# Kernel tuning notes

Measured on AMD Instinct MI355X. Metric: run time of the kernel, lower is better.

The kernel has to match this reference:

```python
import jax, jax.numpy as jnp
import numpy as np

N = 50000      # num nodes
E = 800000     # num edges
D = 128        # num_hid
EPS = 1e-8


def _mlp(x, w1, b1, w2, b2):
    # 2-layer MLP: Linear -> ReLU -> Linear (dropout disabled at inference)
    return jax.nn.relu(x @ w1 + b1) @ w2 + b2


def setup_inputs() -> dict:
    key = jax.random.key(0)
    ks = jax.random.split(key, 12)

    def lin(k, fan_in, fan_out):
        kw, kb = jax.random.split(k)
        lim = 1.0 / np.sqrt(fan_in)
        w = jax.random.uniform(kw, (fan_in, fan_out), jnp.float32, -lim, lim)
        b = jax.random.uniform(kb, (fan_out,), jnp.float32, -lim, lim)
        return w, b

    H = jax.random.normal(ks[0], (N, D), jnp.float32)
    edge_index = jax.random.randint(ks[1], (2, E), 0, N, jnp.int64)
    w1_1, b1_1 = lin(ks[2], 2 * D, D)   # mlp_1 layer 1
    w1_2, b1_2 = lin(ks[3], D, D)       # mlp_1 layer 2
    w2_1, b2_1 = lin(ks[4], 2 * D, D)   # mlp_2 layer 1
    w2_2, b2_2 = lin(ks[5], D, 1)       # mlp_2 layer 2 (channel_curv=False -> out=1)
    t = jnp.zeros((), jnp.float32)
    return {"t": t, "H": H, "edge_index": edge_index,
            "w1_1": w1_1, "b1_1": b1_1, "w1_2": w1_2, "b1_2": b1_2,
            "w2_1": w2_1, "b2_1": b2_1, "w2_2": w2_2, "b2_2": b2_2}


def reference(t, H, edge_index, w1_1, b1_1, w1_2, b1_2, w2_1, b2_1, w2_2, b2_2):
    src, dst = edge_index[0], edge_index[1]

    # damping: row-normalize H
    H = H / (jnp.linalg.norm(H, axis=1, keepdims=True) + EPS)

    H_i = H[src]                                    # [E, D]
    H_j = H[dst]                                    # [E, D]

    # curvature(H_i, H_j)
    c = jnp.concatenate((H_i, H_j), axis=1)         # [E, 2D]
    c = jax.nn.relu(_mlp(c, w1_1, b1_1, w1_2, b1_2))  # [E, D]
    c = jax.ops.segment_sum(c, src, num_segments=N)   # scatter-sum -> [N, D]
    c = jnp.concatenate((c[src], c[dst]), axis=1)     # [E, 2D]
    curv = _mlp(c, w2_1, b2_1, w2_2, b2_2)            # [E, 1]

    # damped edge message
    cos = jnp.sum(H_i * H_j, axis=1, keepdims=True)   # [E, 1]
    H_edge = curv * (H_j - cos * H_i)                 # [E, D]

    # scatter-mean over source node
    s = jax.ops.segment_sum(H_edge, src, num_segments=N)               # [N, D]
    cnt = jax.ops.segment_sum(jnp.ones((E, 1), H.dtype), src, num_segments=N)
    Hm = s / jnp.maximum(cnt, 1.0)

    # damping: row-normalize output
    return Hm / (jnp.linalg.norm(Hm, axis=1, keepdims=True) + EPS)
```

## Files before the change

### kernel.cpp

```cpp
#include <hip/hip_runtime.h>
#include <hip/hip_bf16.h>

#define D 128
#define EPS 1e-8f
#define E1S 136

typedef _Float16 f16;
typedef __attribute__((ext_vector_type(8))) _Float16 half8;
typedef __attribute__((ext_vector_type(4))) float f32x4;
typedef unsigned int uint;

__device__ inline float2 up2(uint u) {
    union { uint u; f16 h[2]; } v; v.u = u;
    return make_float2((float)v.h[0], (float)v.h[1]);
}

__global__ void k_normalize(const float* __restrict__ H, f16* __restrict__ Hn, int N) {
    int row = blockIdx.x * 4 + (threadIdx.x >> 6);
    int lane = threadIdx.x & 63;
    if (row >= N) return;
    float2 v = reinterpret_cast<const float2*>(H + (size_t)row * D)[lane];
    float ss = v.x * v.x + v.y * v.y;
    #pragma unroll
    for (int off = 32; off; off >>= 1) ss += __shfl_xor(ss, off, 64);
    float scale = 1.0f / (sqrtf(ss) + EPS);
    union { f16 h[2]; uint u; } p;
    p.h[0] = (f16)(v.x * scale);
    p.h[1] = (f16)(v.y * scale);
    reinterpret_cast<uint*>(Hn + (size_t)row * D)[lane] = p.u;
}

__global__ void k_hist(const int* __restrict__ src, int* __restrict__ deg, int E) {
    for (int e = blockIdx.x * blockDim.x + threadIdx.x; e < E; e += gridDim.x * blockDim.x)
        atomicAdd(&deg[src[e]], 1);
}

__global__ void k_scan(const int* __restrict__ deg, int* __restrict__ rowptr, int N) {
    __shared__ int wsum[16];
    __shared__ int carry;
    int t = threadIdx.x, lane = t & 63, w = t >> 6;
    if (t == 0) carry = 0;
    __syncthreads();
    for (int base = 0; base < N; base += 4096) {
        int i0 = base + t * 4;
        int a = 0, b = 0, c = 0, d = 0;
        if (i0 + 3 < N) {
            int4 v4 = *reinterpret_cast<const int4*>(deg + i0);
            a = v4.x; b = v4.y; c = v4.z; d = v4.w;
        } else {
            if (i0 < N) a = deg[i0];
            if (i0 + 1 < N) b = deg[i0 + 1];
            if (i0 + 2 < N) c = deg[i0 + 2];
            if (i0 + 3 < N) d = deg[i0 + 3];
        }
        int s1 = a + b, s2 = s1 + c, s3 = s2 + d;
        int v = s3;
        #pragma unroll
        for (int off = 1; off < 64; off <<= 1) {
            int u = __shfl_up(v, off, 64);
            if (lane >= off) v += u;
        }
        if (lane == 63) wsum[w] = v;
        __syncthreads();
        if (w == 0 && lane < 16) {
            int s = wsum[lane];
            #pragma unroll
            for (int off = 1; off < 16; off <<= 1) {
                int u = __shfl_up(s, off, 64);
                if (lane >= off) s += u;
            }
            wsum[lane] = s;
        }
        __syncthreads();
        int add = (w > 0 ? wsum[w - 1] : 0) + carry;
        int incl = v + add;
        int pre = incl - s3;
        if (i0 < N)     rowptr[i0 + 1] = pre + a;
        if (i0 + 1 < N) rowptr[i0 + 2] = pre + s1;
        if (i0 + 2 < N) rowptr[i0 + 3] = pre + s2;
        if (i0 + 3 < N) rowptr[i0 + 4] = pre + s3;
        __syncthreads();
        if (t == 1023) carry = incl;
        __syncthreads();
    }
    if (t == 0) rowptr[0] = 0;
}

__global__ void k_scatter(const int* __restrict__ src, const int* __restrict__ dst,
                          const int* __restrict__ rowptr, int* __restrict__ fill,
                          int* __restrict__ srcS, int* __restrict__ dstS, int E) {
    for (int e = blockIdx.x * blockDim.x + threadIdx.x; e < E; e += gridDim.x * blockDim.x) {
        int s = src[e];
        int pos = atomicAdd(&fill[s], 1);
        int idx = rowptr[s] + pos;
        srcS[idx] = s;
        dstS[idx] = dst[e];
    }
}

__global__ void k_prep_all(const float* __restrict__ w1_1, const float* __restrict__ w1_2,
                           const float* __restrict__ w2_1, f16* __restrict__ Wt) {
    int b = blockIdx.x;
    int m = b >> 6;
    int idx = (b & 63) * 256 + threadIdx.x;
    int k = idx >> 7, n = idx & 127;
    const float* W = (m == 0) ? w1_1
                   : (m == 1) ? w1_1 + 16384
                   : (m == 2) ? w1_2
                   : (m == 3) ? w2_1
                              : w2_1 + 16384;
    Wt[m * 16384 + n * 128 + k] = (f16)W[k * 128 + n];
}

template <bool A_F16>
__global__ __launch_bounds__(256, 4)
void k_gemm_dual(const void* __restrict__ Aptr, const f16* __restrict__ Wt0,
                 const f16* __restrict__ Wt1, const float* __restrict__ bias0,
                 f16* __restrict__ out0, f16* __restrict__ out1, int N) {
    __shared__ f16 As[64 * E1S];
    int t = threadIdx.x;
    int r0 = blockIdx.x * 64;
    int l = t & 63, w = t >> 6, n0 = w * 32;
    {
        int er = t >> 2, kb = (t & 3) * 32;
        int rc = min(r0 + er, N - 1);
        if (A_F16) {
            const half8* Ap = reinterpret_cast<const half8*>((const f16*)Aptr + (size_t)rc * 128 + kb);
            #pragma unroll
            for (int q = 0; q < 4; ++q)
                *reinterpret_cast<half8*>(&As[er * E1S + kb + q * 8]) = Ap[q];
        } else {
            const float4* Ap = reinterpret_cast<const float4*>((const float*)Aptr + (size_t)rc * 128 + kb);
            #pragma unroll
            for (int q = 0; q < 4; ++q) {
                float4 a0 = Ap[q * 2], a1 = Ap[q * 2 + 1];
                half8 sv;
                sv[0] = (f16)a0.x; sv[1] = (f16)a0.y; sv[2] = (f16)a0.z; sv[3] = (f16)a0.w;
                sv[4] = (f16)a1.x; sv[5] = (f16)a1.y; sv[6] = (f16)a1.z; sv[7] = (f16)a1.w;
                *reinterpret_cast<half8*>(&As[er * E1S + kb + q * 8]) = sv;
            }
        }
    }
    half8 bfrag[2][4];
    #pragma unroll
    for (int nt = 0; nt < 2; ++nt) {
        int col = n0 + nt * 16 + (l & 15);
        #pragma unroll
        for (int kt = 0; kt < 4; ++kt)
            bfrag[nt][kt] = *reinterpret_cast<const half8*>(Wt0 + col * 128 + kt * 32 + (l >> 4) * 8);
    }
    float b0a = bias0[n0 + (l & 15)];
    float b0b = bias0[n0 + 16 + (l & 15)];
    __syncthreads();
    f32x4 acc0[4][2], acc1[4][2];
    #pragma unroll
    for (int mt = 0; mt < 4; ++mt) {
        acc0[mt][0] = (f32x4){0,0,0,0}; acc0[mt][1] = (f32x4){0,0,0,0};
        acc1[mt][0] = (f32x4){0,0,0,0}; acc1[mt][1] = (f32x4){0,0,0,0};
    }
    #pragma unroll
    for (int mt = 0; mt < 4; ++mt) {
        int arow = mt * 16 + (l & 15);
        #pragma unroll
        for (int kt = 0; kt < 4; ++kt) {
            half8 af = *reinterpret_cast<const half8*>(&As[arow * E1S + kt * 32 + (l >> 4) * 8]);
            acc0[mt][0] = __builtin_amdgcn_mfma_f32_16x16x32_f16(af, bfrag[0][kt], acc0[mt][0], 0, 0, 0);
            acc0[mt][1] = __builtin_amdgcn_mfma_f32_16x16x32_f16(af, bfrag[1][kt], acc0[mt][1], 0, 0, 0);
        }
    }
    #pragma unroll
    for (int nt = 0; nt < 2; ++nt) {
        int col = n0 + nt * 16 + (l & 15);
        #pragma unroll
        for (int kt = 0; kt < 4; ++kt)
            bfrag[nt][kt] = *reinterpret_cast<const half8*>(Wt1 + col * 128 + kt * 32 + (l >> 4) * 8);
    }
    #pragma unroll
    for (int mt = 0; mt < 4; ++mt) {
        int arow = mt * 16 + (l & 15);
        #pragma unroll
        for (int kt = 0; kt < 4; ++kt) {
            half8 af = *reinterpret_cast<const half8*>(&As[arow * E1S + kt * 32 + (l >> 4) * 8]);
            acc1[mt][0] = __builtin_amdgcn_mfma_f32_16x16x32_f16(af, bfrag[0][kt], acc1[mt][0], 0, 0, 0);
            acc1[mt][1] = __builtin_amdgcn_mfma_f32_16x16x32_f16(af, bfrag[1][kt], acc1[mt][1], 0, 0, 0);
        }
    }
    __syncthreads();
    #pragma unroll
    for (int mt = 0; mt < 4; ++mt)
        #pragma unroll
        for (int j = 0; j < 4; ++j) {
            int row = mt * 16 + (l >> 4) * 4 + j;
            As[row * E1S + n0 + (l & 15)]      = (f16)(acc0[mt][0][j] + b0a);
            As[row * E1S + n0 + 16 + (l & 15)] = (f16)(acc0[mt][1][j] + b0b);
        }
    __syncthreads();
    {
        int er = t >> 2, kb = (t & 3) * 32;
        int row = r0 + er;
        if (row < N)
            #pragma unroll
            for (int q = 0; q < 4; ++q)
                *reinterpret_cast<half8*>(out0 + (size_t)row * 128 + kb + q * 8) =
                    *reinterpret_cast<const half8*>(&As[er * E1S + kb + q * 8]);
    }
    __syncthreads();
    #pragma unroll
    for (int mt = 0; mt < 4; ++mt)
        #pragma unroll
        for (int j = 0; j < 4; ++j) {
            int row = mt * 16 + (l >> 4) * 4 + j;
            As[row * E1S + n0 + (l & 15)]      = (f16)acc1[mt][0][j];
            As[row * E1S + n0 + 16 + (l & 15)] = (f16)acc1[mt][1][j];
        }
    __syncthreads();
    {
        int er = t >> 2, kb = (t & 3) * 32;
        int row = r0 + er;
        if (row < N)
            #pragma unroll
            for (int q = 0; q < 4; ++q)
                *reinterpret_cast<half8*>(out1 + (size_t)row * 128 + kb + q * 8) =
                    *reinterpret_cast<const half8*>(&As[er * E1S + kb + q * 8]);
    }
}

__global__ __launch_bounds__(256, 5)
void k_edge_mlp1(const int* __restrict__ srcS, const int* __restrict__ dstS,
                 const int* __restrict__ rowptr,
                 const f16* __restrict__ P, const f16* __restrict__ Q,
                 const f16* __restrict__ Wt, const float* __restrict__ b1_2,
                 float* __restrict__ C, int E) {
    __shared__ f16 e1s[64 * E1S];
    int t = threadIdx.x;
    int e0 = blockIdx.x * 64;
    int l = t & 63, w = t >> 6, n0 = w * 32;
    {
        int er = t >> 2, kb = (t & 3) * 32;
        int ge = min(e0 + er, E - 1);
        int sc = srcS[ge], dj = dstS[ge];
        const half8* Pp = reinterpret_cast<const half8*>(P + (size_t)sc * 128 + kb);
        const half8* Qp = reinterpret_cast<const half8*>(Q + (size_t)dj * 128 + kb);
        #pragma unroll
        for (int q = 0; q < 4; ++q) {
            half8 sv = Pp[q] + Qp[q];
            #pragma unroll
            for (int i = 0; i < 8; ++i)
                sv[i] = sv[i] > (f16)0 ? sv[i] : (f16)0;
            *reinterpret_cast<half8*>(&e1s[er * E1S + kb + q * 8]) = sv;
        }
    }
    half8 bfrag[2][4];
    #pragma unroll
    for (int nt = 0; nt < 2; ++nt) {
        int col = n0 + nt * 16 + (l & 15);
        #pragma unroll
        for (int kt = 0; kt < 4; ++kt)
            bfrag[nt][kt] = *reinterpret_cast<const half8*>(Wt + col * 128 + kt * 32 + (l >> 4) * 8);
    }
    float bias0 = b1_2[n0 + (l & 15)];
    float bias1 = b1_2[n0 + 16 + (l & 15)];
    __syncthreads();
    f32x4 acc[4][2];
    #pragma unroll
    for (int mt = 0; mt < 4; ++mt) { acc[mt][0] = (f32x4){0,0,0,0}; acc[mt][1] = (f32x4){0,0,0,0}; }
    #pragma unroll
    for (int mt = 0; mt < 4; ++mt) {
        int arow = mt * 16 + (l & 15);
        #pragma unroll
        for (int kt = 0; kt < 4; ++kt) {
            half8 af = *reinterpret_cast<const half8*>(&e1s[arow * E1S + kt * 32 + (l >> 4) * 8]);
            acc[mt][0] = __builtin_amdgcn_mfma_f32_16x16x32_f16(af, bfrag[0][kt], acc[mt][0], 0, 0, 0);
            acc[mt][1] = __builtin_amdgcn_mfma_f32_16x16x32_f16(af, bfrag[1][kt], acc[mt][1], 0, 0, 0);
        }
    }
    #pragma unroll
    for (int mt = 0; mt < 4; ++mt)
        #pragma unroll
        for (int j = 0; j < 4; ++j) {
            acc[mt][0][j] = fmaxf(acc[mt][0][j] + bias0, 0.f);
            acc[mt][1][j] = fmaxf(acc[mt][1][j] + bias1, 0.f);
        }
    int myv = (e0 + l < E) ? srcS[e0 + l] : -1;
    int pv = __shfl_up(myv, 1, 64);
    bool head = (l == 0) || (myv != pv);
    unsigned long long validm = __ballot(myv >= 0);
    unsigned long long hm = __ballot(head) & validm;
    int nvalid = __popcll(validm);
    int grp = l >> 4;
    while (hm) {
        int lo = __builtin_ctzll(hm);
        hm &= hm - 1;
        int hi = hm ? __builtin_ctzll(hm) : nvalid;
        int s = __shfl(myv, lo, 64);
        float v0 = 0.f, v1 = 0.f;
        #pragma unroll
        for (int mt = 0; mt < 4; ++mt) {
            int tlo = mt * 16, thi = mt * 16 + 16;
            if (thi <= lo || tlo >= hi) continue;
            if (lo <= tlo && hi >= thi) {
                #pragma unroll
                for (int j = 0; j < 4; ++j) {
                    v0 += acc[mt][0][j];
                    v1 += acc[mt][1][j];
                }
            } else {
                #pragma unroll
                for (int j = 0; j < 4; ++j) {
                    int row = tlo + grp * 4 + j;
                    bool in = (row >= lo) && (row < hi);
                    v0 += in ? acc[mt][0][j] : 0.f;
                    v1 += in ? acc[mt][1][j] : 0.f;
                }
            }
        }
        v0 += __shfl_xor(v0, 16, 64); v0 += __shfl_xor(v0, 32, 64);
        v1 += __shfl_xor(v1, 16, 64); v1 += __shfl_xor(v1, 32, 64);
        if (l < 16) {
            int rs = rowptr[s], re = rowptr[s + 1];
            float* cp = C + (size_t)s * 128 + n0 + l;
            if (rs >= e0 && re <= e0 + 64) {
                cp[0] = v0; cp[16] = v1;
            } else {
                atomicAdd(cp, v0); atomicAdd(cp + 16, v1);
            }
        }
    }
}

__global__ void k_node_curv(const int* __restrict__ dstS, const int* __restrict__ rowptr,
                            const f16* __restrict__ Hn,
                            const f16* __restrict__ Rb, const f16* __restrict__ Tb,
                            const float* __restrict__ w2_2, const float* __restrict__ b2_2,
                            float* __restrict__ out, int N) {
    int node = blockIdx.x * 4 + (threadIdx.x >> 6);
    int lane = threadIdx.x & 63;
    if (node >= N) return;
    int sub = lane & 15;
    int slot = lane >> 4;
    const uint4* HnU = reinterpret_cast<const uint4*>(Hn);
    const uint4* TbU = reinterpret_cast<const uint4*>(Tb);
    uint4 hiu = HnU[(size_t)node * 16 + sub];
    uint4 rvu = reinterpret_cast<const uint4*>(Rb)[(size_t)node * 16 + sub];
    float hif[8], rvf[8], wvf[8];
    {
        const uint* hp = &hiu.x;
        const uint* rp = &rvu.x;
        float4 w0 = reinterpret_cast<const float4*>(w2_2)[sub * 2];
        float4 w1 = reinterpret_cast<const float4*>(w2_2)[sub * 2 + 1];
        #pragma unroll
        for (int k = 0; k < 4; ++k) {
            float2 h = up2(hp[k]); hif[k * 2] = h.x; hif[k * 2 + 1] = h.y;
            float2 r = up2(rp[k]); rvf[k * 2] = r.x; rvf[k * 2 + 1] = r.y;
        }
        wvf[0] = w0.x; wvf[1] = w0.y; wvf[2] = w0.z; wvf[3] = w0.w;
        wvf[4] = w1.x; wvf[5] = w1.y; wvf[6] = w1.z; wvf[7] = w1.w;
    }
    float bb = b2_2[0];
    int lo = rowptr[node], hiE = rowptr[node + 1];
    int deg = hiE - lo;
    float ax[8];
    #pragma unroll
    for (int j = 0; j < 8; ++j) ax[j] = 0.f;
    float sc = 0.f;
    int e = lo + slot;
    bool valid = e < hiE;
    int dcur = valid ? dstS[e] : 0;
    uint4 hju = HnU[(size_t)dcur * 16 + sub];
    uint4 tvu = TbU[(size_t)dcur * 16 + sub];
    for (int it = 0; it < deg; it += 4) {
        int e2 = lo + it + 4 + slot;
        bool valid2 = e2 < hiE;
        int d2 = valid2 ? dstS[e2] : 0;
        uint4 hjN = HnU[(size_t)d2 * 16 + sub];
        uint4 tvN = TbU[(size_t)d2 * 16 + sub];
        float hjf[8];
        float pcos = 0.f, pcur = 0.f;
        {
            const uint* hp = &hju.x;
            const uint* tp = &tvu.x;
            #pragma unroll
            for (int k = 0; k < 4; ++k) {
                float2 h = up2(hp[k]);
                float2 tv = up2(tp[k]);
                hjf[k * 2] = h.x; hjf[k * 2 + 1] = h.y;
                pcos += hif[k * 2] * h.x + hif[k * 2 + 1] * h.y;
                pcur += fmaxf(rvf[k * 2] + tv.x, 0.f) * wvf[k * 2]
                      + fmaxf(rvf[k * 2 + 1] + tv.y, 0.f) * wvf[k * 2 + 1];
            }
        }
        #pragma unroll
        for (int off = 1; off < 16; off <<= 1) {
            pcos += __shfl_xor(pcos, off, 64);
            pcur += __shfl_xor(pcur, off, 64);
        }
        float cur = valid ? (pcur + bb) : 0.f;
        #pragma unroll
        for (int j = 0; j < 8; ++j) ax[j] += cur * hjf[j];
        sc += cur * pcos;
        hju = hjN; tvu = tvN; valid = valid2;
    }
    #pragma unroll
    for (int j = 0; j < 8; ++j) {
        ax[j] += __shfl_xor(ax[j], 16, 64);
        ax[j] += __shfl_xor(ax[j], 32, 64);
    }
    sc += __shfl_xor(sc, 16, 64);
    sc += __shfl_xor(sc, 32, 64);
    float inv = 1.0f / fmaxf((float)deg, 1.0f);
    float ss = 0.f;
    #pragma unroll
    for (int j = 0; j < 8; ++j) {
        ax[j] = (ax[j] - sc * hif[j]) * inv;
        ss += ax[j] * ax[j];
    }
    #pragma unroll
    for (int off = 1; off < 16; off <<= 1) ss += __shfl_xor(ss, off, 64);
    float scale = 1.0f / (sqrtf(ss) + EPS);
    if (slot == 0) {
        float4 o0 = make_float4(ax[0] * scale, ax[1] * scale, ax[2] * scale, ax[3] * scale);
        float4 o1 = make_float4(ax[4] * scale, ax[5] * scale, ax[6] * scale, ax[7] * scale);
        float4* op = reinterpret_cast<float4*>(out + (size_t)node * 128 + sub * 8);
        op[0] = o0;
        op[1] = o1;
    }
}

extern "C" void kernel_launch(void* const* d_in, const int* in_sizes, int n_in,
                              void* d_out, int out_size, void* d_ws, size_t ws_size,
                              hipStream_t stream) {
    const float* H    = (const float*)d_in[1];
    const int*   ei   = (const int*)d_in[2];
    const float* w1_1 = (const float*)d_in[3];
    const float* b1_1 = (const float*)d_in[4];
    const float* w1_2 = (const float*)d_in[5];
    const float* b1_2 = (const float*)d_in[6];
    const float* w2_1 = (const float*)d_in[7];
    const float* b2_1 = (const float*)d_in[8];
    const float* w2_2 = (const float*)d_in[9];
    const float* b2_2 = (const float*)d_in[10];

    int N = in_sizes[1] / D;
    int E = in_sizes[2] / 2;
    const int* src = ei;
    const int* dst = ei + E;

    float* out = (float*)d_out;

    f16* Hnb    = (f16*)d_ws;
    f16* Pb     = Hnb + (size_t)N * D;
    f16* Qb     = Pb + (size_t)N * D;
    float* Cb   = (float*)(Qb + (size_t)N * D);
    f16* Wt     = (f16*)(Cb + (size_t)N * D);
    int* deg    = (int*)(Wt + 5 * 16384);
    int* rowptr = deg + N;
    int* fill   = rowptr + N + 1;
    int* srcS   = fill + N;
    int* dstS   = srcS + E;

    hipMemsetAsync(Cb, 0, (size_t)N * D * sizeof(float), stream);
    hipMemsetAsync(deg, 0, (3 * (size_t)N + 1) * sizeof(int), stream);

    k_normalize<<<(N + 3) / 4, 256, 0, stream>>>(H, Hnb, N);
    k_hist<<<1024, 256, 0, stream>>>(src, deg, E);
    k_scan<<<1, 1024, 0, stream>>>(deg, rowptr, N);
    k_scatter<<<1024, 256, 0, stream>>>(src, dst, rowptr, fill, srcS, dstS, E);
    k_prep_all<<<320, 256, 0, stream>>>(w1_1, w1_2, w2_1, Wt);

    k_gemm_dual<true><<<(N + 63) / 64, 256, 0, stream>>>(Hnb, Wt + 0 * 16384, Wt + 1 * 16384,
                                                         b1_1, Pb, Qb, N);
    k_edge_mlp1<<<(E + 63) / 64, 256, 0, stream>>>(srcS, dstS, rowptr, Pb, Qb,
                                                   Wt + 2 * 16384, b1_2, Cb, E);
    k_gemm_dual<false><<<(N + 63) / 64, 256, 0, stream>>>(Cb, Wt + 3 * 16384, Wt + 4 * 16384,
                                                          b2_1, Pb, Qb, N);
    k_node_curv<<<(N + 3) / 4, 256, 0, stream>>>(dstS, rowptr, Hnb, Pb, Qb, w2_2, b2_2, out, N);
}
```

Measured before the change: 352.4 us.

## Interleave normalized H with T rows and double-tile edge MLP blocks

Normalized H and the second-layer T projection are now stored interleaved in one 256-wide row buffer. The per-edge gather in k_node_curv can then fetch both halves for a destination node from one contiguous 512-byte region instead of two separate arrays. Separately, k_edge_mlp1 processes two 64-edge tiles per block, gathering the second tile into registers while the first is computed. This hides gather latency, at the cost of more registers and LDS and lower occupancy (launch bounds 5 to 4).

```diff
diff --git a/kernel.cpp b/kernel.cpp
--- a/kernel.cpp
+++ b/kernel.cpp
@@ -15,7 +15,7 @@
     return make_float2((float)v.h[0], (float)v.h[1]);
 }
 
-__global__ void k_normalize(const float* __restrict__ H, f16* __restrict__ Hn, int N) {
+__global__ void k_normalize(const float* __restrict__ H, f16* __restrict__ HT, int N) {
     int row = blockIdx.x * 4 + (threadIdx.x >> 6);
     int lane = threadIdx.x & 63;
     if (row >= N) return;
@@ -27,7 +27,7 @@
     union { f16 h[2]; uint u; } p;
     p.h[0] = (f16)(v.x * scale);
     p.h[1] = (f16)(v.y * scale);
-    reinterpret_cast<uint*>(Hn + (size_t)row * D)[lane] = p.u;
+    reinterpret_cast<uint*>(HT + (size_t)row * 256)[lane] = p.u;
 }
 
 __global__ void k_hist(const int* __restrict__ src, int* __restrict__ deg, int E) {
@@ -116,7 +116,8 @@
 __global__ __launch_bounds__(256, 4)
 void k_gemm_dual(const void* __restrict__ Aptr, const f16* __restrict__ Wt0,
                  const f16* __restrict__ Wt1, const float* __restrict__ bias0,
-                 f16* __restrict__ out0, f16* __restrict__ out1, int N) {
+                 f16* __restrict__ out0, f16* __restrict__ out1, int N,
+                 int astr, int o1str) {
     __shared__ f16 As[64 * E1S];
     int t = threadIdx.x;
     int r0 = blockIdx.x * 64;
@@ -125,12 +126,12 @@
         int er = t >> 2, kb = (t & 3) * 32;
         int rc = min(r0 + er, N - 1);
         if (A_F16) {
-            const half8* Ap = reinterpret_cast<const half8*>((const f16*)Aptr + (size_t)rc * 128 + kb);
+            const half8* Ap = reinterpret_cast<const half8*>((const f16*)Aptr + (size_t)rc * astr + kb);
             #pragma unroll
             for (int q = 0; q < 4; ++q)
                 *reinterpret_cast<half8*>(&As[er * E1S + kb + q * 8]) = Ap[q];
         } else {
-            const float4* Ap = reinterpret_cast<const float4*>((const float*)Aptr + (size_t)rc * 128 + kb);
+            const float4* Ap = reinterpret_cast<const float4*>((const float*)Aptr + (size_t)rc * astr + kb);
             #pragma unroll
             for (int q = 0; q < 4; ++q) {
                 float4 a0 = Ap[q * 2], a1 = Ap[q * 2 + 1];
@@ -220,24 +221,26 @@
         if (row < N)
             #pragma unroll
             for (int q = 0; q < 4; ++q)
-                *reinterpret_cast<half8*>(out1 + (size_t)row * 128 + kb + q * 8) =
+                *reinterpret_cast<half8*>(out1 + (size_t)row * o1str + kb + q * 8) =
                     *reinterpret_cast<const half8*>(&As[er * E1S + kb + q * 8]);
     }
 }
 
-__global__ __launch_bounds__(256, 5)
+__global__ __launch_bounds__(256, 4)
 void k_edge_mlp1(const int* __restrict__ srcS, const int* __restrict__ dstS,
                  const int* __restrict__ rowptr,
                  const f16* __restrict__ P, const f16* __restrict__ Q,
                  const f16* __restrict__ Wt, const float* __restrict__ b1_2,
                  float* __restrict__ C, int E) {
-    __shared__ f16 e1s[64 * E1S];
+    __shared__ f16 e1s[2 * 64 * E1S];
     int t = threadIdx.x;
-    int e0 = blockIdx.x * 64;
+    int e00 = blockIdx.x * 128;
+    int e01 = e00 + 64;
     int l = t & 63, w = t >> 6, n0 = w * 32;
+    int er = t >> 2, kb = (t & 3) * 32;
+
     {
-        int er = t >> 2, kb = (t & 3) * 32;
-        int ge = min(e0 + er, E - 1);
+        int ge = min(e00 + er, E - 1);
         int sc = srcS[ge], dj = dstS[ge];
         const half8* Pp = reinterpret_cast<const half8*>(P + (size_t)sc * 128 + kb);
         const half8* Qp = reinterpret_cast<const half8*>(Q + (size_t)dj * 128 + kb);
@@ -250,6 +253,21 @@
             *reinterpret_cast<half8*>(&e1s[er * E1S + kb + q * 8]) = sv;
         }
     }
+    half8 sv1[4];
+    {
+        int ge = min(e01 + er, E - 1);
+        int sc = srcS[ge], dj = dstS[ge];
+        const half8* Pp = reinterpret_cast<const half8*>(P + (size_t)sc * 128 + kb);
+        const half8* Qp = reinterpret_cast<const half8*>(Q + (size_t)dj * 128 + kb);
+        #pragma unroll
+        for (int q = 0; q < 4; ++q) {
+            half8 sv = Pp[q] + Qp[q];
+            #pragma unroll
+            for (int i = 0; i < 8; ++i)
+                sv[i] = sv[i] > (f16)0 ? sv[i] : (f16)0;
+            sv1[q] = sv;
+        }
+    }
     half8 bfrag[2][4];
     #pragma unroll
     for (int nt = 0; nt < 2; ++nt) {
@@ -260,77 +278,86 @@
     }
     float bias0 = b1_2[n0 + (l & 15)];
     float bias1 = b1_2[n0 + 16 + (l & 15)];
-    __syncthreads();
-    f32x4 acc[4][2];
-    #pragma unroll
-    for (int mt = 0; mt < 4; ++mt) { acc[mt][0] = (f32x4){0,0,0,0}; acc[mt][1] = (f32x4){0,0,0,0}; }
-    #pragma unroll
-    for (int mt = 0; mt < 4; ++mt) {
-        int arow = mt * 16 + (l & 15);
-        #pragma unroll
-        for (int kt = 0; kt < 4; ++kt) {
-            half8 af = *reinterpret_cast<const half8*>(&e1s[arow * E1S + kt * 32 + (l >> 4) * 8]);
-            acc[mt][0] = __builtin_amdgcn_mfma_f32_16x16x32_f16(af, bfrag[0][kt], acc[mt][0], 0, 0, 0);
-            acc[mt][1] = __builtin_amdgcn_mfma_f32_16x16x32_f16(af, bfrag[1][kt], acc[mt][1], 0, 0, 0);
-        }
-    }
-    #pragma unroll
-    for (int mt = 0; mt < 4; ++mt)
-        #pragma unroll
-        for (int j = 0; j < 4; ++j) {
-            acc[mt][0][j] = fmaxf(acc[mt][0][j] + bias0, 0.f);
-            acc[mt][1][j] = fmaxf(acc[mt][1][j] + bias1, 0.f);
-        }
-    int myv = (e0 + l < E) ? srcS[e0 + l] : -1;
-    int pv = __shfl_up(myv, 1, 64);
-    bool head = (l == 0) || (myv != pv);
-    unsigned long long validm = __ballot(myv >= 0);
-    unsigned long long hm = __ballot(head) & validm;
-    int nvalid = __popcll(validm);
-    int grp = l >> 4;
-    while (hm) {
-        int lo = __builtin_ctzll(hm);
-        hm &= hm - 1;
-        int hi = hm ? __builtin_ctzll(hm) : nvalid;
-        int s = __shfl(myv, lo, 64);
-        float v0 = 0.f, v1 = 0.f;
+
+    auto compute_tile = [&](const f16* buf, int ebase) {
+        f32x4 acc[4][2];
+        #pragma unroll
+        for (int mt = 0; mt < 4; ++mt) { acc[mt][0] = (f32x4){0,0,0,0}; acc[mt][1] = (f32x4){0,0,0,0}; }
         #pragma unroll
         for (int mt = 0; mt < 4; ++mt) {
-            int tlo = mt * 16, thi = mt * 16 + 16;
-            if (thi <= lo || tlo >= hi) continue;
-            if (lo <= tlo && hi >= thi) {
-                #pragma unroll
-                for (int j = 0; j < 4; ++j) {
-                    v0 += acc[mt][0][j];
-                    v1 += acc[mt][1][j];
+            int arow = mt * 16 + (l & 15);
+            #pragma unroll
+            for (int kt = 0; kt < 4; ++kt) {
+                half8 af = *reinterpret_cast<const half8*>(&buf[arow * E1S + kt * 32 + (l >> 4) * 8]);
+                acc[mt][0] = __builtin_amdgcn_mfma_f32_16x16x32_f16(af, bfrag[0][kt], acc[mt][0], 0, 0, 0);
+                acc[mt][1] = __builtin_amdgcn_mfma_f32_16x16x32_f16(af, bfrag[1][kt], acc[mt][1], 0, 0, 0);
+            }
+        }
+        #pragma unroll
+        for (int mt = 0; mt < 4; ++mt)
+            #pragma unroll
+            for (int j = 0; j < 4; ++j) {
+                acc[mt][0][j] = fmaxf(acc[mt][0][j] + bias0, 0.f);
+                acc[mt][1][j] = fmaxf(acc[mt][1][j] + bias1, 0.f);
+            }
+        int myv = (ebase + l < E) ? srcS[ebase + l] : -1;
+        int pvv = __shfl_up(myv, 1, 64);
+        bool head = (l == 0) || (myv != pvv);
+        unsigned long long validm = __ballot(myv >= 0);
+        unsigned long long hm = __ballot(head) & validm;
+        int nvalid = __popcll(validm);
+        int grp = l >> 4;
+        while (hm) {
+            int lo = __builtin_ctzll(hm);
+            hm &= hm - 1;
+            int hi = hm ? __builtin_ctzll(hm) : nvalid;
+            int s = __shfl(myv, lo, 64);
+            float v0 = 0.f, v1 = 0.f;
+            #pragma unroll
+            for (int mt = 0; mt < 4; ++mt) {
+                int tlo = mt * 16, thi = mt * 16 + 16;
+                if (thi <= lo || tlo >= hi) continue;
+                if (lo <= tlo && hi >= thi) {
+                    #pragma unroll
+                    for (int j = 0; j < 4; ++j) {
+                        v0 += acc[mt][0][j];
+                        v1 += acc[mt][1][j];
+                    }
+                } else {
+                    #pragma unroll
+                    for (int j = 0; j < 4; ++j) {
+                        int row = tlo + grp * 4 + j;
+                        bool in = (row >= lo) && (row < hi);
+                        v0 += in ? acc[mt][0][j] : 0.f;
+                        v1 += in ? acc[mt][1][j] : 0.f;
+                    }
                 }
-            } else {
-                #pragma unroll
-                for (int j = 0; j < 4; ++j) {
-                    int row = tlo + grp * 4 + j;
-                    bool in = (row >= lo) && (row < hi);
-                    v0 += in ? acc[mt][0][j] : 0.f;
-                    v1 += in ? acc[mt][1][j] : 0.f;
+            }
+            v0 += __shfl_xor(v0, 16, 64); v0 += __shfl_xor(v0, 32, 64);
+            v1 += __shfl_xor(v1, 16, 64); v1 += __shfl_xor(v1, 32, 64);
+            if (l < 16) {
+                int rs = rowptr[s], re = rowptr[s + 1];
+                float* cp = C + (size_t)s * 128 + n0 + l;
+                if (rs >= ebase && re <= ebase + 64) {
+                    cp[0] = v0; cp[16] = v1;
+                } else {
+                    atomicAdd(cp, v0); atomicAdd(cp + 16, v1);
                 }
             }
         }
-        v0 += __shfl_xor(v0, 16, 64); v0 += __shfl_xor(v0, 32, 64);
-        v1 += __shfl_xor(v1, 16, 64); v1 += __shfl_xor(v1, 32, 64);
-        if (l < 16) {
-            int rs = rowptr[s], re = rowptr[s + 1];
-            float* cp = C + (size_t)s * 128 + n0 + l;
-            if (rs >= e0 && re <= e0 + 64) {
-                cp[0] = v0; cp[16] = v1;
-            } else {
-                atomicAdd(cp, v0); atomicAdd(cp + 16, v1);
-            }
-        }
-    }
+    };
+
+    __syncthreads();
+    compute_tile(e1s, e00);
+    #pragma unroll
+    for (int q = 0; q < 4; ++q)
+        *reinterpret_cast<half8*>(&e1s[64 * E1S + er * E1S + kb + q * 8]) = sv1[q];
+    __syncthreads();
+    compute_tile(e1s + 64 * E1S, e01);
 }
 
 __global__ void k_node_curv(const int* __restrict__ dstS, const int* __restrict__ rowptr,
-                            const f16* __restrict__ Hn,
-                            const f16* __restrict__ Rb, const f16* __restrict__ Tb,
+                            const f16* __restrict__ HT, const f16* __restrict__ Rb,
                             const float* __restrict__ w2_2, const float* __restrict__ b2_2,
                             float* __restrict__ out, int N) {
     int node = blockIdx.x * 4 + (threadIdx.x >> 6);
@@ -338,9 +365,8 @@
     if (node >= N) return;
     int sub = lane & 15;
     int slot = lane >> 4;
-    const uint4* HnU = reinterpret_cast<const uint4*>(Hn);
-    const uint4* TbU = reinterpret_cast<const uint4*>(Tb);
-    uint4 hiu = HnU[(size_t)node * 16 + sub];
+    const uint4* HTU = reinterpret_cast<const uint4*>(HT);
+    uint4 hiu = HTU[(size_t)node * 32 + sub];
     uint4 rvu = reinterpret_cast<const uint4*>(Rb)[(size_t)node * 16 + sub];
     float hif[8], rvf[8], wvf[8];
     {
@@ -366,14 +392,14 @@
     int e = lo + slot;
     bool valid = e < hiE;
     int dcur = valid ? dstS[e] : 0;
-    uint4 hju = HnU[(size_t)dcur * 16 + sub];
-    uint4 tvu = TbU[(size_t)dcur * 16 + sub];
+    uint4 hju = HTU[(size_t)dcur * 32 + sub];
+    uint4 tvu = HTU[(size_t)dcur * 32 + 16 + sub];
     for (int it = 0; it < deg; it += 4) {
         int e2 = lo + it + 4 + slot;
         bool valid2 = e2 < hiE;
         int d2 = valid2 ? dstS[e2] : 0;
-        uint4 hjN = HnU[(size_t)d2 * 16 + sub];
-        uint4 tvN = TbU[(size_t)d2 * 16 + sub];
+        uint4 hjN = HTU[(size_t)d2 * 32 + sub];
+        uint4 tvN = HTU[(size_t)d2 * 32 + 16 + sub];
         float hjf[8];
         float pcos = 0.f, pcur = 0.f;
         {
@@ -447,8 +473,8 @@
 
     float* out = (float*)d_out;
 
-    f16* Hnb    = (f16*)d_ws;
-    f16* Pb     = Hnb + (size_t)N * D;
+    f16* HT     = (f16*)d_ws;
+    f16* Pb     = HT + (size_t)N * 256;
     f16* Qb     = Pb + (size_t)N * D;
     float* Cb   = (float*)(Qb + (size_t)N * D);
     f16* Wt     = (f16*)(Cb + (size_t)N * D);
@@ -461,17 +487,17 @@
     hipMemsetAsync(Cb, 0, (size_t)N * D * sizeof(float), stream);
     hipMemsetAsync(deg, 0, (3 * (size_t)N + 1) * sizeof(int), stream);
 
-    k_normalize<<<(N + 3) / 4, 256, 0, stream>>>(H, Hnb, N);
+    k_normalize<<<(N + 3) / 4, 256, 0, stream>>>(H, HT, N);
     k_hist<<<1024, 256, 0, stream>>>(src, deg, E);
     k_scan<<<1, 1024, 0, stream>>>(deg, rowptr, N);
     k_scatter<<<1024, 256, 0, stream>>>(src, dst, rowptr, fill, srcS, dstS, E);
     k_prep_all<<<320, 256, 0, stream>>>(w1_1, w1_2, w2_1, Wt);
 
-    k_gemm_dual<true><<<(N + 63) / 64, 256, 0, stream>>>(Hnb, Wt + 0 * 16384, Wt + 1 * 16384,
-                                                         b1_1, Pb, Qb, N);
-    k_edge_mlp1<<<(E + 63) / 64, 256, 0, stream>>>(srcS, dstS, rowptr, Pb, Qb,
-                                                   Wt + 2 * 16384, b1_2, Cb, E);
+    k_gemm_dual<true><<<(N + 63) / 64, 256, 0, stream>>>(HT, Wt + 0 * 16384, Wt + 1 * 16384,
+                                                         b1_1, Pb, Qb, N, 256, 128);
+    k_edge_mlp1<<<(E + 127) / 128, 256, 0, stream>>>(srcS, dstS, rowptr, Pb, Qb,
+                                                     Wt + 2 * 16384, b1_2, Cb, E);
     k_gemm_dual<false><<<(N + 63) / 64, 256, 0, stream>>>(Cb, Wt + 3 * 16384, Wt + 4 * 16384,
-                                                          b2_1, Pb, Qb, N);
-    k_node_curv<<<(N + 3) / 4, 256, 0, stream>>>(dstS, rowptr, Hnb, Pb, Qb, w2_2, b2_2, out, N);
-}
+                                                          b2_1, Pb, HT + 128, N, 128, 256);
+    k_node_curv<<<(N + 3) / 4, 256, 0, stream>>>(dstS, rowptr, HT, Pb, w2_2, b2_2, out, N);
+}
```

After: 354.5 us. Within noise of the previous version (+0.6%).

## Fuse prologue kernels and interleave Hn with Tb rows for node_curv gathers

Applied to the files above, without the earlier changes.

Merges normalize, degree histogram and weight transpose into one launch using block-range dispatch, removing two kernel launches. Stores the normalized H and the second GEMM's Tb output interleaved in a single 256-wide f16 row buffer, so node_curv's per-neighbor gathers of Hn and Tb hit one contiguous 512-byte row instead of two separate arrays. GEMM kernels gain stride parameters to read and write the interleaved layout.

```diff
diff --git a/kernel.cpp b/kernel.cpp
--- a/kernel.cpp
+++ b/kernel.cpp
@@ -15,24 +15,42 @@
     return make_float2((float)v.h[0], (float)v.h[1]);
 }
 
-__global__ void k_normalize(const float* __restrict__ H, f16* __restrict__ Hn, int N) {
-    int row = blockIdx.x * 4 + (threadIdx.x >> 6);
-    int lane = threadIdx.x & 63;
-    if (row >= N) return;
-    float2 v = reinterpret_cast<const float2*>(H + (size_t)row * D)[lane];
-    float ss = v.x * v.x + v.y * v.y;
-    #pragma unroll
-    for (int off = 32; off; off >>= 1) ss += __shfl_xor(ss, off, 64);
-    float scale = 1.0f / (sqrtf(ss) + EPS);
-    union { f16 h[2]; uint u; } p;
-    p.h[0] = (f16)(v.x * scale);
-    p.h[1] = (f16)(v.y * scale);
-    reinterpret_cast<uint*>(Hn + (size_t)row * D)[lane] = p.u;
-}
-
-__global__ void k_hist(const int* __restrict__ src, int* __restrict__ deg, int E) {
-    for (int e = blockIdx.x * blockDim.x + threadIdx.x; e < E; e += gridDim.x * blockDim.x)
-        atomicAdd(&deg[src[e]], 1);
+__global__ void k_prologue(const float* __restrict__ H, f16* __restrict__ HT,
+                           const int* __restrict__ src, int* __restrict__ deg,
+                           const float* __restrict__ w1_1, const float* __restrict__ w1_2,
+                           const float* __restrict__ w2_1, f16* __restrict__ Wt,
+                           int N, int E, int nbN) {
+    int b = blockIdx.x;
+    int t = threadIdx.x;
+    if (b < nbN) {
+        int row = b * 4 + (t >> 6);
+        int lane = t & 63;
+        if (row >= N) return;
+        float2 v = reinterpret_cast<const float2*>(H + (size_t)row * D)[lane];
+        float ss = v.x * v.x + v.y * v.y;
+        #pragma unroll
+        for (int off = 32; off; off >>= 1) ss += __shfl_xor(ss, off, 64);
+        float scale = 1.0f / (sqrtf(ss) + EPS);
+        union { f16 h[2]; uint u; } p;
+        p.h[0] = (f16)(v.x * scale);
+        p.h[1] = (f16)(v.y * scale);
+        reinterpret_cast<uint*>(HT + (size_t)row * 256)[lane] = p.u;
+    } else if (b < nbN + 1024) {
+        int bb = b - nbN;
+        for (int e = bb * 256 + t; e < E; e += 1024 * 256)
+            atomicAdd(&deg[src[e]], 1);
+    } else {
+        int bb = b - nbN - 1024;
+        int m = bb >> 6;
+        int idx = (bb & 63) * 256 + t;
+        int k = idx >> 7, n = idx & 127;
+        const float* W = (m == 0) ? w1_1
+                       : (m == 1) ? w1_1 + 16384
+                       : (m == 2) ? w1_2
+                       : (m == 3) ? w2_1
+                                  : w2_1 + 16384;
+        Wt[m * 16384 + n * 128 + k] = (f16)W[k * 128 + n];
+    }
 }
 
 __global__ void k_scan(const int* __restrict__ deg, int* __restrict__ rowptr, int N) {
@@ -98,25 +116,12 @@
     }
 }
 
-__global__ void k_prep_all(const float* __restrict__ w1_1, const float* __restrict__ w1_2,
-                           const float* __restrict__ w2_1, f16* __restrict__ Wt) {
-    int b = blockIdx.x;
-    int m = b >> 6;
-    int idx = (b & 63) * 256 + threadIdx.x;
-    int k = idx >> 7, n = idx & 127;
-    const float* W = (m == 0) ? w1_1
-                   : (m == 1) ? w1_1 + 16384
-                   : (m == 2) ? w1_2
-                   : (m == 3) ? w2_1
-                              : w2_1 + 16384;
-    Wt[m * 16384 + n * 128 + k] = (f16)W[k * 128 + n];
-}
-
 template <bool A_F16>
 __global__ __launch_bounds__(256, 4)
 void k_gemm_dual(const void* __restrict__ Aptr, const f16* __restrict__ Wt0,
                  const f16* __restrict__ Wt1, const float* __restrict__ bias0,
-                 f16* __restrict__ out0, f16* __restrict__ out1, int N) {
+                 f16* __restrict__ out0, f16* __restrict__ out1, int N,
+                 int astr, int o1str) {
     __shared__ f16 As[64 * E1S];
     int t = threadIdx.x;
     int r0 = blockIdx.x * 64;
@@ -125,12 +130,12 @@
         int er = t >> 2, kb = (t & 3) * 32;
         int rc = min(r0 + er, N - 1);
         if (A_F16) {
-            const half8* Ap = reinterpret_cast<const half8*>((const f16*)Aptr + (size_t)rc * 128 + kb);
+            const half8* Ap = reinterpret_cast<const half8*>((const f16*)Aptr + (size_t)rc * astr + kb);
             #pragma unroll
             for (int q = 0; q < 4; ++q)
                 *reinterpret_cast<half8*>(&As[er * E1S + kb + q * 8]) = Ap[q];
         } else {
-            const float4* Ap = reinterpret_cast<const float4*>((const float*)Aptr + (size_t)rc * 128 + kb);
+            const float4* Ap = reinterpret_cast<const float4*>((const float*)Aptr + (size_t)rc * astr + kb);
             #pragma unroll
             for (int q = 0; q < 4; ++q) {
                 float4 a0 = Ap[q * 2], a1 = Ap[q * 2 + 1];
@@ -220,7 +225,7 @@
         if (row < N)
             #pragma unroll
             for (int q = 0; q < 4; ++q)
-                *reinterpret_cast<half8*>(out1 + (size_t)row * 128 + kb + q * 8) =
+                *reinterpret_cast<half8*>(out1 + (size_t)row * o1str + kb + q * 8) =
                     *reinterpret_cast<const half8*>(&As[er * E1S + kb + q * 8]);
     }
 }
@@ -329,8 +334,7 @@
 }
 
 __global__ void k_node_curv(const int* __restrict__ dstS, const int* __restrict__ rowptr,
-                            const f16* __restrict__ Hn,
-                            const f16* __restrict__ Rb, const f16* __restrict__ Tb,
+                            const f16* __restrict__ HT, const f16* __restrict__ Rb,
                             const float* __restrict__ w2_2, const float* __restrict__ b2_2,
                             float* __restrict__ out, int N) {
     int node = blockIdx.x * 4 + (threadIdx.x >> 6);
@@ -338,9 +342,8 @@
     if (node >= N) return;
     int sub = lane & 15;
     int slot = lane >> 4;
-    const uint4* HnU = reinterpret_cast<const uint4*>(Hn);
-    const uint4* TbU = reinterpret_cast<const uint4*>(Tb);
-    uint4 hiu = HnU[(size_t)node * 16 + sub];
+    const uint4* HTU = reinterpret_cast<const uint4*>(HT);
+    uint4 hiu = HTU[(size_t)node * 32 + sub];
     uint4 rvu = reinterpret_cast<const uint4*>(Rb)[(size_t)node * 16 + sub];
     float hif[8], rvf[8], wvf[8];
     {
@@ -366,14 +369,14 @@
     int e = lo + slot;
     bool valid = e < hiE;
     int dcur = valid ? dstS[e] : 0;
-    uint4 hju = HnU[(size_t)dcur * 16 + sub];
-    uint4 tvu = TbU[(size_t)dcur * 16 + sub];
+    uint4 hju = HTU[(size_t)dcur * 32 + sub];
+    uint4 tvu = HTU[(size_t)dcur * 32 + 16 + sub];
     for (int it = 0; it < deg; it += 4) {
         int e2 = lo + it + 4 + slot;
         bool valid2 = e2 < hiE;
         int d2 = valid2 ? dstS[e2] : 0;
-        uint4 hjN = HnU[(size_t)d2 * 16 + sub];
-        uint4 tvN = TbU[(size_t)d2 * 16 + sub];
+        uint4 hjN = HTU[(size_t)d2 * 32 + sub];
+        uint4 tvN = HTU[(size_t)d2 * 32 + 16 + sub];
         float hjf[8];
         float pcos = 0.f, pcur = 0.f;
         {
@@ -447,8 +450,8 @@
 
     float* out = (float*)d_out;
 
-    f16* Hnb    = (f16*)d_ws;
-    f16* Pb     = Hnb + (size_t)N * D;
+    f16* HT     = (f16*)d_ws;
+    f16* Pb     = HT + (size_t)N * 256;
     f16* Qb     = Pb + (size_t)N * D;
     float* Cb   = (float*)(Qb + (size_t)N * D);
     f16* Wt     = (f16*)(Cb + (size_t)N * D);
@@ -461,17 +464,17 @@
     hipMemsetAsync(Cb, 0, (size_t)N * D * sizeof(float), stream);
     hipMemsetAsync(deg, 0, (3 * (size_t)N + 1) * sizeof(int), stream);
 
-    k_normalize<<<(N + 3) / 4, 256, 0, stream>>>(H, Hnb, N);
-    k_hist<<<1024, 256, 0, stream>>>(src, deg, E);
+    int nbN = (N + 3) / 4;
+    k_prologue<<<nbN + 1024 + 320, 256, 0, stream>>>(H, HT, src, deg,
+                                                     w1_1, w1_2, w2_1, Wt, N, E, nbN);
     k_scan<<<1, 1024, 0, stream>>>(deg, rowptr, N);
     k_scatter<<<1024, 256, 0, stream>>>(src, dst, rowptr, fill, srcS, dstS, E);
-    k_prep_all<<<320, 256, 0, stream>>>(w1_1, w1_2, w2_1, Wt);
-
-    k_gemm_dual<true><<<(N + 63) / 64, 256, 0, stream>>>(Hnb, Wt + 0 * 16384, Wt + 1 * 16384,
-                                                         b1_1, Pb, Qb, N);
+
+    k_gemm_dual<true><<<(N + 63) / 64, 256, 0, stream>>>(HT, Wt + 0 * 16384, Wt + 1 * 16384,
+                                                         b1_1, Pb, Qb, N, 256, 128);
     k_edge_mlp1<<<(E + 63) / 64, 256, 0, stream>>>(srcS, dstS, rowptr, Pb, Qb,
                                                    Wt + 2 * 16384, b1_2, Cb, E);
     k_gemm_dual<false><<<(N + 63) / 64, 256, 0, stream>>>(Cb, Wt + 3 * 16384, Wt + 4 * 16384,
-                                                          b2_1, Pb, Qb, N);
-    k_node_curv<<<(N + 3) / 4, 256, 0, stream>>>(dstS, rowptr, Hnb, Pb, Qb, w2_2, b2_2, out, N);
-}
+                                                          b2_1, Pb, HT + 128, N, 128, 256);
+    k_node_curv<<<(N + 3) / 4, 256, 0, stream>>>(dstS, rowptr, HT, Pb, w2_2, b2_2, out, N);
+}
```

Measured after the change: 345.9 us. Within noise of the previous version (-1.8%).
